# Performance work log

Hardware: AMD Instinct MI355X
Metric: run time of the kernel (lower is better)

## Reference

```python
import jax, jax.numpy as jnp
import numpy as np

EPS = 1e-12  # torch F.normalize default eps


def setup_inputs() -> dict:
    key = jax.random.key(0)
    k1, k2, k3, k4, k5 = jax.random.split(key, 5)
    N, E, D_IN, D_OUT = 100000, 1600000, 128, 128
    features = jax.random.normal(k1, (N, D_IN), dtype=jnp.float32)
    W = jax.random.normal(k2, (D_OUT, D_IN), dtype=jnp.float32) * 0.05
    b = jax.random.normal(k3, (D_OUT,), dtype=jnp.float32) * 0.05
    src = jax.random.randint(k4, (E,), 0, N, dtype=jnp.int32)
    dst = jax.random.randint(k5, (E,), 0, N, dtype=jnp.int32)
    return {"features": features, "W": W, "b": b, "src": src, "dst": dst}


def reference(features, W, b, src, dst):
    N = features.shape[0]
    # sum of features over each node's neighbors: scatter-add messages to dst
    neigh_sum = jax.ops.segment_sum(features[src], dst, num_segments=N)  # [N, D]
    total = jnp.sum(features, axis=0)  # [D]
    # non-neighbor sum (excl. self) + self feature == total - neighbor_sum
    h_NN = total[None, :] - neigh_sum  # [N, D]
    # row-wise L2 normalize (torch F.normalize dim=1)
    norm = jnp.sqrt(jnp.sum(h_NN * h_NN, axis=1, keepdims=True))
    h_norm = h_NN / jnp.maximum(norm, EPS)
    # linear: x @ W.T + b
    return h_norm @ W.T + b
```

## Files before the change

### kernel.cpp

```cpp
#include <hip/hip_runtime.h>
#include <hip/hip_bf16.h>

#define D 128
#define FS_CAP 5120

typedef __bf16 bf16_t;
typedef bf16_t bf16x8 __attribute__((ext_vector_type(8)));
typedef float  f32x4  __attribute__((ext_vector_type(4)));
typedef float  f32x2  __attribute__((ext_vector_type(2)));

__device__ __forceinline__ void atomAddF(float* p, float v) {
    unsafeAtomicAdd(p, v);
}

__device__ __forceinline__ uint2 pack_fp8x8(const float* v) {
    unsigned lo = 0, hi = 0;
    lo = __builtin_amdgcn_cvt_pk_fp8_f32(v[0], v[1], lo, false);
    lo = __builtin_amdgcn_cvt_pk_fp8_f32(v[2], v[3], lo, true);
    hi = __builtin_amdgcn_cvt_pk_fp8_f32(v[4], v[5], hi, false);
    hi = __builtin_amdgcn_cvt_pk_fp8_f32(v[6], v[7], hi, true);
    return make_uint2(lo, hi);
}

__device__ __forceinline__ void acc_fp8x8(uint2 w, float* acc) {
    f32x2 a = __builtin_amdgcn_cvt_pk_f32_fp8(w.x, false);
    f32x2 b = __builtin_amdgcn_cvt_pk_f32_fp8(w.x, true);
    f32x2 c = __builtin_amdgcn_cvt_pk_f32_fp8(w.y, false);
    f32x2 d = __builtin_amdgcn_cvt_pk_f32_fp8(w.y, true);
    acc[0] += a[0]; acc[1] += a[1]; acc[2] += b[0]; acc[3] += b[1];
    acc[4] += c[0]; acc[5] += c[1]; acc[6] += d[0]; acc[7] += d[1];
}

__global__ __launch_bounds__(256) void cvt_colsum_count_kernel(const float* __restrict__ feat,
                                                               uint2* __restrict__ featq,
                                                               float* __restrict__ total,
                                                               const int* __restrict__ dst,
                                                               int* __restrict__ bcount,
                                                               int* __restrict__ chunkhist,
                                                               long long n8, int nE, int NB,
                                                               int echunk) {
    __shared__ float red[4][16][8];
    __shared__ int hist[1024];
    int tid = threadIdx.x, lane = tid & 63, w = tid >> 6;
    for (int i = tid; i < NB; i += 256) hist[i] = 0;
    __syncthreads();
    long long G = (long long)gridDim.x * 256;
    float acc[8];
    #pragma unroll
    for (int e = 0; e < 8; ++e) acc[e] = 0.f;
    int c0 = blockIdx.x * echunk;
    int c1 = c0 + echunk; if (c1 > nE) c1 = nE;
    long long i = (long long)blockIdx.x * 256 + tid;
    int e = c0 + tid;
    while (i < n8 || e < c1) {
        if (i < n8) {
            const float4 a = *(const float4*)&feat[i * 8];
            const float4 b = *(const float4*)&feat[i * 8 + 4];
            float v[8] = {a.x, a.y, a.z, a.w, b.x, b.y, b.z, b.w};
            featq[i] = pack_fp8x8(v);
            acc[0] += a.x; acc[1] += a.y; acc[2] += a.z; acc[3] += a.w;
            acc[4] += b.x; acc[5] += b.y; acc[6] += b.z; acc[7] += b.w;
        }
        if (e < c1) atomicAdd(&hist[dst[e] >> 8], 1);
        i += G; e += 256;
    }
    #pragma unroll
    for (int k = 0; k < 8; ++k) {
        acc[k] += __shfl_xor(acc[k], 16, 64);
        acc[k] += __shfl_xor(acc[k], 32, 64);
    }
    if (lane < 16) {
        #pragma unroll
        for (int k = 0; k < 8; ++k) red[w][lane][k] = acc[k];
    }
    __syncthreads();
    if (tid < 128) {
        int cb = tid >> 3, k = tid & 7;
        float s = red[0][cb][k] + red[1][cb][k] + red[2][cb][k] + red[3][cb][k];
        atomAddF(&total[cb * 8 + k], s);
    }
    int* ch = chunkhist + (size_t)(blockIdx.x >> 2) * 1024;
    for (int k = tid; k < NB; k += 256) {
        int h = hist[k];
        if (h) { atomicAdd(&ch[k], h); atomicAdd(&bcount[k], h); }
    }
}

__global__ __launch_bounds__(1024) void bucket_scatter_kernel(const int* __restrict__ src,
                                                              const int* __restrict__ dst,
                                                              const int* __restrict__ bcount,
                                                              int* __restrict__ bcur_rel,
                                                              int* __restrict__ bbase,
                                                              unsigned* __restrict__ packed,
                                                              const int* __restrict__ chunkhist,
                                                              int nE, int NB, int echunk4) {
    __shared__ int ws[16];
    __shared__ int cur[1024];
    int blk = blockIdx.x;
    int tid = threadIdx.x, lane = tid & 63, w = tid >> 6;

    int v = (tid < NB) ? bcount[tid] : 0;
    int x = v;
    #pragma unroll
    for (int off = 1; off < 64; off <<= 1) {
        int y = __shfl_up(x, off, 64);
        if (lane >= off) x += y;
    }
    if (lane == 63) ws[w] = x;
    __syncthreads();
    if (w == 0 && lane < 16) {
        int s = ws[lane];
        #pragma unroll
        for (int off = 1; off < 16; off <<= 1) {
            int y = __shfl_up(s, off, 64);
            if (lane >= off) s += y;
        }
        ws[lane] = s;
    }
    __syncthreads();
    int base = (w == 0) ? 0 : ws[w - 1];
    int excl = base + x - v;

    if (blk == 0) {
        if (tid < NB) bbase[tid] = excl;
        if (tid == 0) bbase[NB] = nE;
    }
    if (tid < NB) {
        int h = chunkhist[(size_t)blk * 1024 + tid];
        cur[tid] = h ? (excl + atomicAdd(&bcur_rel[tid], h)) : 0;
    }
    __syncthreads();

    int c0 = blk * echunk4;
    int c1 = c0 + echunk4; if (c1 > nE) c1 = nE;
    for (int i = c0 + tid; i < c1; i += 1024) {
        int t = dst[i];
        int b = t >> 8;
        int off = atomicAdd(&cur[b], 1);
        packed[off] = ((unsigned)(t & 255) << 17) | (unsigned)src[i];
    }
}

__global__ __launch_bounds__(1024) void fill_sort_kernel(const unsigned* __restrict__ packed,
                                                         const int* __restrict__ bbase,
                                                         int* __restrict__ ptr,
                                                         int* __restrict__ adj,
                                                         int n, int NB, int nE) {
    __shared__ int cnt[256];
    __shared__ int lcur[256];
    __shared__ int wsum[4];
    __shared__ int pbuf[FS_CAP];
    __shared__ int sbuf[FS_CAP];
    int b = blockIdx.x;
    int tid = threadIdx.x, lane = tid & 63, w = tid >> 6;
    int base = bbase[b], end = bbase[b + 1], m = end - base;
    bool fast = (m <= FS_CAP);
    if (tid < 256) cnt[tid] = 0;
    __syncthreads();
    if (fast) {
        for (int i = tid; i < m; i += 1024) {
            int pv = (int)packed[base + i];
            pbuf[i] = pv;
            atomicAdd(&cnt[pv >> 17], 1);
        }
    } else {
        for (int i = tid; i < m; i += 1024)
            atomicAdd(&cnt[packed[base + i] >> 17], 1);
    }
    __syncthreads();
    int v = 0, x = 0;
    if (tid < 256) {
        v = cnt[tid];
        x = v;
        #pragma unroll
        for (int off = 1; off < 64; off <<= 1) {
            int y = __shfl_up(x, off, 64);
            if (lane >= off) x += y;
        }
        if (lane == 63) wsum[w] = x;
    }
    __syncthreads();
    if (tid < 256) {
        int wb = 0;
        for (int k = 0; k < w; ++k) wb += wsum[k];
        int excl = wb + x - v;
        lcur[tid] = fast ? excl : base + excl;
        int node = b * 256 + tid;
        if (node < n) ptr[node] = base + excl;
    }
    if (b == NB - 1 && tid == 0) ptr[n] = nE;
    __syncthreads();
    if (fast) {
        for (int i = tid; i < m; i += 1024) {
            int pv = pbuf[i];
            int j = pv >> 17;
            int pos = atomicAdd(&lcur[j], 1);
            sbuf[pos] = pv & 0x1FFFF;
        }
        __syncthreads();
        for (int i = tid; i < m; i += 1024)
            adj[base + i] = sbuf[i];
    } else {
        for (int i = tid; i < m; i += 1024) {
            int pv = (int)packed[base + i];
            int j = pv >> 17;
            int pos = atomicAdd(&lcur[j], 1);
            adj[pos] = pv & 0x1FFFF;
        }
    }
}

__global__ __launch_bounds__(256, 4) void gather_mfma_kernel(const uint2* __restrict__ featq,
                                                             const int* __restrict__ ptr,
                                                             const int* __restrict__ adj,
                                                             const float* __restrict__ total,
                                                             const float* __restrict__ W,
                                                             const float* __restrict__ bias,
                                                             float* __restrict__ out,
                                                             int n, int ngroups) {
    __shared__ bf16_t s_hn[2][16][136];

    int tid  = threadIdx.x;
    int lane = tid & 63;
    int w    = tid >> 6;
    int quad = lane >> 4;
    int l16  = lane & 15;

    int n0 = w * 32;
    bf16x8 bfrag[4][2];
    #pragma unroll
    for (int s = 0; s < 4; ++s)
        #pragma unroll
        for (int c = 0; c < 2; ++c) {
            const float* wp = W + (size_t)(n0 + 16 * c + l16) * D + 32 * s + 8 * quad;
            float4 wa = *(const float4*)wp;
            float4 wb = *(const float4*)(wp + 4);
            bf16x8 bf;
            bf[0] = (bf16_t)wa.x; bf[1] = (bf16_t)wa.y; bf[2] = (bf16_t)wa.z; bf[3] = (bf16_t)wa.w;
            bf[4] = (bf16_t)wb.x; bf[5] = (bf16_t)wb.y; bf[6] = (bf16_t)wb.z; bf[7] = (bf16_t)wb.w;
            bfrag[s][c] = bf;
        }
    float bias0 = bias[n0 + l16];
    float bias1 = bias[n0 + 16 + l16];

    int k_node = tid >> 4;
    int d8 = (tid & 15) * 8;
    float tot8[8];
    {
        float4 ta = *(const float4*)&total[d8];
        float4 tb = *(const float4*)&total[d8 + 4];
        tot8[0] = ta.x; tot8[1] = ta.y; tot8[2] = ta.z; tot8[3] = ta.w;
        tot8[4] = tb.x; tot8[5] = tb.y; tot8[6] = tb.z; tot8[7] = tb.w;
    }

    unsigned sliceoff = (unsigned)(tid & 15) * 8;
    unsigned long long fbase = (unsigned long long)featq;
    int pb = 0;
    int gstride = gridDim.x;
    int g = blockIdx.x;

    int p0 = 0, p1 = 0, madj = 0;
    if (g < ngroups) {
        int v = g * 16 + k_node;
        if (v < n) { p0 = ptr[v]; p1 = ptr[v + 1]; }
        if (p0 < p1) { int q = p0 + l16; if (q > p1 - 1) q = p1 - 1; madj = adj[q]; }
    }

    for (; g < ngroups; g += gstride) {
        int gn = g + gstride;
        int np0 = 0, np1 = 0;
        if (gn < ngroups) {
            int vn = gn * 16 + k_node;
            if (vn < n) { np0 = ptr[vn]; np1 = ptr[vn + 1]; }
        }

        float acc8[8];
        #pragma unroll
        for (int e = 0; e < 8; ++e) acc8[e] = 0.f;

        for (int p = p0; p < p1; p += 16) {
            int rem = p1 - p;
            unsigned voff[16];
            #pragma unroll
            for (int i = 0; i < 16; ++i) {
                int idx = __shfl(madj, (lane & 48) + i, 64);
                voff[i] = ((unsigned)idx << 7) | sliceoff;
            }
            uint2 f[16];
            #pragma unroll
            for (int i = 0; i < 16; ++i)
                asm volatile("global_load_dwordx2 %0, %1, %2"
                             : "=v"(f[i]) : "v"(voff[i]), "s"(fbase));
            int adjn = 0, pn = p + 16;
            if (pn < p1) { int q = pn + l16; if (q > p1 - 1) q = p1 - 1; adjn = adj[q]; }
            asm volatile("s_waitcnt vmcnt(8)" ::: "memory");
            __builtin_amdgcn_sched_barrier(0);
            #pragma unroll
            for (int i = 0; i < 8; ++i) if (i < rem) acc_fp8x8(f[i], acc8);
            asm volatile("s_waitcnt vmcnt(0)" ::: "memory");
            __builtin_amdgcn_sched_barrier(0);
            #pragma unroll
            for (int i = 8; i < 16; ++i) if (i < rem) acc_fp8x8(f[i], acc8);
            madj = adjn;
        }

        int v = g * 16 + k_node;
        bool valid = v < n;
        float h8[8], ss = 0.f;
        #pragma unroll
        for (int e = 0; e < 8; ++e) {
            h8[e] = valid ? (tot8[e] - acc8[e]) : 0.f;
            ss = fmaf(h8[e], h8[e], ss);
        }
        ss += __shfl_xor(ss, 1, 64);
        ss += __shfl_xor(ss, 2, 64);
        ss += __shfl_xor(ss, 4, 64);
        ss += __shfl_xor(ss, 8, 64);
        float rinv = 1.0f / fmaxf(sqrtf(ss), 1e-12f);

        bf16x8 hv;
        #pragma unroll
        for (int e = 0; e < 8; ++e) hv[e] = (bf16_t)(h8[e] * rinv);
        *(bf16x8*)&s_hn[pb][k_node][d8] = hv;
        __syncthreads();

        p0 = np0; p1 = np1; madj = 0;
        if (p0 < p1) { int q = p0 + l16; if (q > p1 - 1) q = p1 - 1; madj = adj[q]; }

        f32x4 acc0 = {0.f, 0.f, 0.f, 0.f};
        f32x4 acc1 = {0.f, 0.f, 0.f, 0.f};
        #pragma unroll
        for (int s = 0; s < 4; ++s) {
            bf16x8 a = *(const bf16x8*)&s_hn[pb][l16][32 * s + 8 * quad];
            acc0 = __builtin_amdgcn_mfma_f32_16x16x32_bf16(a, bfrag[s][0], acc0, 0, 0, 0);
            acc1 = __builtin_amdgcn_mfma_f32_16x16x32_bf16(a, bfrag[s][1], acc1, 0, 0, 0);
        }
        #pragma unroll
        for (int r = 0; r < 4; ++r) {
            int row = quad * 4 + r;
            int vr = g * 16 + row;
            if (vr < n) {
                out[(size_t)vr * D + n0 + l16]      = acc0[r] + bias0;
                out[(size_t)vr * D + n0 + 16 + l16] = acc1[r] + bias1;
            }
        }
        pb ^= 1;
    }
}

__global__ __launch_bounds__(128) void col_sum_kernel(const float* __restrict__ feat,
                                                      float* __restrict__ total, int n) {
    int d = threadIdx.x;
    float acc = 0.f;
    for (int r = blockIdx.x; r < n; r += gridDim.x)
        acc += feat[(size_t)r * D + d];
    atomAddF(&total[d], acc);
}

__global__ __launch_bounds__(256) void scatter_kernel(const float* __restrict__ feat,
                                                      const int* __restrict__ src,
                                                      const int* __restrict__ dst,
                                                      float* __restrict__ neigh, int nE) {
    long long nwork = (long long)nE * 64;
    long long stride = (long long)gridDim.x * 256;
    for (long long i = (long long)blockIdx.x * 256 + threadIdx.x; i < nwork; i += stride) {
        int e = (int)(i >> 6);
        int d2 = (int)(i & 63) * 2;
        int s = src[e], t = dst[e];
        const float2 vv = *(const float2*)&feat[(size_t)s * D + d2];
        float* p = &neigh[(size_t)t * D + d2];
        atomAddF(p + 0, vv.x);
        atomAddF(p + 1, vv.y);
    }
}

__global__ __launch_bounds__(256) void finalize_kernel(const float* __restrict__ neigh,
                                                       const float* __restrict__ total,
                                                       const float* __restrict__ W,
                                                       const float* __restrict__ bias,
                                                       float* __restrict__ out,
                                                       int n, int ngroups) {
    __shared__ __hip_bfloat16 Wt[D * D];
    __shared__ __align__(16) float hnt[2][D][4];
    __shared__ float red[2][2][4];
    int tid = threadIdx.x;
    for (int idx = tid; idx < D * D; idx += 256) {
        int j = idx & 127, dd = idx >> 7;
        Wt[idx] = __float2bfloat16(W[(size_t)j * D + dd]);
    }
    int half = tid >> 7, d = tid & 127, wih = (tid >> 6) & 1, lane = tid & 63;
    float bj = bias[d], tot = total[d];
    __syncthreads();
    for (int g = blockIdx.x; g < ngroups; g += gridDim.x) {
        int nb = g * 8 + half * 4;
        float h0=0,h1=0,h2=0,h3=0;
        if (nb+0 < n) h0 = tot - neigh[(size_t)(nb+0)*D + d];
        if (nb+1 < n) h1 = tot - neigh[(size_t)(nb+1)*D + d];
        if (nb+2 < n) h2 = tot - neigh[(size_t)(nb+2)*D + d];
        if (nb+3 < n) h3 = tot - neigh[(size_t)(nb+3)*D + d];
        float s0=h0*h0,s1=h1*h1,s2=h2*h2,s3=h3*h3;
        #pragma unroll
        for (int off = 32; off > 0; off >>= 1) {
            s0 += __shfl_xor(s0, off, 64); s1 += __shfl_xor(s1, off, 64);
            s2 += __shfl_xor(s2, off, 64); s3 += __shfl_xor(s3, off, 64);
        }
        if (lane == 0) { red[half][wih][0]=s0; red[half][wih][1]=s1; red[half][wih][2]=s2; red[half][wih][3]=s3; }
        __syncthreads();
        float rinv[4];
        #pragma unroll
        for (int k = 0; k < 4; ++k)
            rinv[k] = 1.0f / fmaxf(sqrtf(red[half][0][k] + red[half][1][k]), 1e-12f);
        hnt[half][d][0]=h0*rinv[0]; hnt[half][d][1]=h1*rinv[1];
        hnt[half][d][2]=h2*rinv[2]; hnt[half][d][3]=h3*rinv[3];
        __syncthreads();
        float a0=0,a1=0,a2=0,a3=0;
        #pragma unroll 8
        for (int dd = 0; dd < D; ++dd) {
            float4 hn4 = *(const float4*)&hnt[half][dd][0];
            float wv = __bfloat162float(Wt[dd * D + d]);
            a0 = fmaf(hn4.x, wv, a0); a1 = fmaf(hn4.y, wv, a1);
            a2 = fmaf(hn4.z, wv, a2); a3 = fmaf(hn4.w, wv, a3);
        }
        if (nb+0 < n) out[(size_t)(nb+0)*D + d] = a0 + bj;
        if (nb+1 < n) out[(size_t)(nb+1)*D + d] = a1 + bj;
        if (nb+2 < n) out[(size_t)(nb+2)*D + d] = a2 + bj;
        if (nb+3 < n) out[(size_t)(nb+3)*D + d] = a3 + bj;
        __syncthreads();
    }
}

static inline size_t align_up(size_t x, size_t a) { return (x + a - 1) & ~(a - 1); }

extern "C" void kernel_launch(void* const* d_in, const int* in_sizes, int n_in,
                              void* d_out, int out_size, void* d_ws, size_t ws_size,
                              hipStream_t stream) {
    const float* feat = (const float*)d_in[0];
    const float* W    = (const float*)d_in[1];
    const float* bias = (const float*)d_in[2];
    const int*   src  = (const int*)d_in[3];
    const int*   dst  = (const int*)d_in[4];
    float* out = (float*)d_out;

    int n  = in_sizes[0] / D;
    int nE = in_sizes[3];
    int NB = (n + 255) / 256;

    char* wsb = (char*)d_ws;
    size_t o_total  = 0;
    size_t o_bcount = 512;
    size_t o_bcurr  = 512 + 4096;
    size_t o_chist  = o_bcurr + 4096;
    size_t o_bbase  = o_chist + (size_t)128 * 1024 * 4;
    size_t o_ptr    = align_up(o_bbase + 4608, 512);
    size_t o_adj    = align_up(o_ptr + (size_t)4 * (n + 1), 512);
    size_t o_packed = o_adj + (size_t)4 * nE;
    size_t o_featq  = align_up(o_packed + (size_t)4 * nE, 512);
    size_t needNew  = o_featq + (size_t)n * D;

    float*    total  = (float*)(wsb + o_total);
    int*      bcount = (int*)(wsb + o_bcount);
    int*      bcurr  = (int*)(wsb + o_bcurr);
    int*      chist  = (int*)(wsb + o_chist);
    int*      bbase  = (int*)(wsb + o_bbase);
    int*      ptr    = (int*)(wsb + o_ptr);
    int*      adj    = (int*)(wsb + o_adj);
    unsigned* packed = (unsigned*)(wsb + o_packed);
    uint2*    featq  = (uint2*)(wsb + o_featq);

    long long n8 = (long long)n * (D / 8);
    int ngroups16 = (n + 15) / 16;
    int grid16 = (ngroups16 + 1) / 2;
    if (grid16 > 16384) grid16 = 16384;

    bool packOK = (n <= (1 << 17)) && (NB <= 1024);

    if (ws_size >= needNew && packOK) {
        hipMemsetAsync(wsb, 0, o_bbase, stream);
        int echunk = (nE + 511) / 512;
        int echunk4 = echunk * 4;
        cvt_colsum_count_kernel<<<512, 256, 0, stream>>>(feat, featq, total, dst, bcount,
                                                         chist, n8, nE, NB, echunk);
        bucket_scatter_kernel<<<128, 1024, 0, stream>>>(src, dst, bcount, bcurr, bbase,
                                                        packed, chist, nE, NB, echunk4);
        fill_sort_kernel<<<NB, 1024, 0, stream>>>(packed, bbase, ptr, adj, n, NB, nE);
        gather_mfma_kernel<<<grid16, 256, 0, stream>>>(featq, ptr, adj, total, W,
                                                       bias, out, n, ngroups16);
    } else {
        float* neigh = out;
        if (ws_size >= D * sizeof(float))
            hipMemsetAsync(d_ws, 0, D * sizeof(float), stream);
        hipMemsetAsync(neigh, 0, (size_t)out_size * sizeof(float), stream);
        col_sum_kernel<<<512, 128, 0, stream>>>(feat, total, n);
        scatter_kernel<<<16384, 256, 0, stream>>>(feat, src, dst, neigh, nE);
        int ngroups = (n + 7) / 8;
        finalize_kernel<<<2048, 256, 0, stream>>>(neigh, total, W, bias, out, n, ngroups);
    }
}
```

Baseline: 211.5 us.

## Split fused convert/colsum/count kernel into separate count and convert kernels

Splits the combined fp8-conversion, column-sum and dst-bucket histogram kernel into a dedicated bucket_count kernel and a standalone cvt_colsum kernel. The convert kernel now runs with 2048 blocks, the count and scatter kernels with 256 blocks. Each count block writes its own chunk histogram directly instead of four blocks atomically merging into a shared one, so the workspace is rearranged so that chist is no longer covered by the zeroing memset. The goal is to remove the imbalance of the fused loop and the global atomics, at the cost of one extra kernel launch and a larger chunk-histogram buffer.

Result: slower. 248.1 us (+17.3%).

```diff
diff --git a/kernel.cpp b/kernel.cpp
--- a/kernel.cpp
+++ b/kernel.cpp
@@ -31,38 +31,23 @@
     acc[4] += c[0]; acc[5] += c[1]; acc[6] += d[0]; acc[7] += d[1];
 }
 
-__global__ __launch_bounds__(256) void cvt_colsum_count_kernel(const float* __restrict__ feat,
-                                                               uint2* __restrict__ featq,
-                                                               float* __restrict__ total,
-                                                               const int* __restrict__ dst,
-                                                               int* __restrict__ bcount,
-                                                               int* __restrict__ chunkhist,
-                                                               long long n8, int nE, int NB,
-                                                               int echunk) {
+__global__ __launch_bounds__(256) void cvt_colsum_kernel(const float* __restrict__ feat,
+                                                         uint2* __restrict__ featq,
+                                                         float* __restrict__ total,
+                                                         long long n8) {
     __shared__ float red[4][16][8];
-    __shared__ int hist[1024];
     int tid = threadIdx.x, lane = tid & 63, w = tid >> 6;
-    for (int i = tid; i < NB; i += 256) hist[i] = 0;
-    __syncthreads();
     long long G = (long long)gridDim.x * 256;
     float acc[8];
     #pragma unroll
     for (int e = 0; e < 8; ++e) acc[e] = 0.f;
-    int c0 = blockIdx.x * echunk;
-    int c1 = c0 + echunk; if (c1 > nE) c1 = nE;
-    long long i = (long long)blockIdx.x * 256 + tid;
-    int e = c0 + tid;
-    while (i < n8 || e < c1) {
-        if (i < n8) {
-            const float4 a = *(const float4*)&feat[i * 8];
-            const float4 b = *(const float4*)&feat[i * 8 + 4];
-            float v[8] = {a.x, a.y, a.z, a.w, b.x, b.y, b.z, b.w};
-            featq[i] = pack_fp8x8(v);
-            acc[0] += a.x; acc[1] += a.y; acc[2] += a.z; acc[3] += a.w;
-            acc[4] += b.x; acc[5] += b.y; acc[6] += b.z; acc[7] += b.w;
-        }
-        if (e < c1) atomicAdd(&hist[dst[e] >> 8], 1);
-        i += G; e += 256;
+    for (long long i = (long long)blockIdx.x * 256 + tid; i < n8; i += G) {
+        const float4 a = *(const float4*)&feat[i * 8];
+        const float4 b = *(const float4*)&feat[i * 8 + 4];
+        float v[8] = {a.x, a.y, a.z, a.w, b.x, b.y, b.z, b.w};
+        featq[i] = pack_fp8x8(v);
+        acc[0] += a.x; acc[1] += a.y; acc[2] += a.z; acc[3] += a.w;
+        acc[4] += b.x; acc[5] += b.y; acc[6] += b.z; acc[7] += b.w;
     }
     #pragma unroll
     for (int k = 0; k < 8; ++k) {
@@ -79,10 +64,25 @@
         float s = red[0][cb][k] + red[1][cb][k] + red[2][cb][k] + red[3][cb][k];
         atomAddF(&total[cb * 8 + k], s);
     }
-    int* ch = chunkhist + (size_t)(blockIdx.x >> 2) * 1024;
+}
+
+__global__ __launch_bounds__(256) void bucket_count_kernel(const int* __restrict__ dst,
+                                                           int* __restrict__ bcount,
+                                                           int* __restrict__ chunkhist,
+                                                           int nE, int NB, int echunkS) {
+    __shared__ int hist[1024];
+    int tid = threadIdx.x;
+    for (int i = tid; i < NB; i += 256) hist[i] = 0;
+    __syncthreads();
+    int c0 = blockIdx.x * echunkS;
+    int c1 = c0 + echunkS; if (c1 > nE) c1 = nE;
+    for (int i = c0 + tid; i < c1; i += 256) atomicAdd(&hist[dst[i] >> 8], 1);
+    __syncthreads();
+    int* ch = chunkhist + (size_t)blockIdx.x * 1024;
     for (int k = tid; k < NB; k += 256) {
         int h = hist[k];
-        if (h) { atomicAdd(&ch[k], h); atomicAdd(&bcount[k], h); }
+        ch[k] = h;
+        if (h) atomicAdd(&bcount[k], h);
     }
 }
 
@@ -93,7 +93,7 @@
                                                               int* __restrict__ bbase,
                                                               unsigned* __restrict__ packed,
                                                               const int* __restrict__ chunkhist,
-                                                              int nE, int NB, int echunk4) {
+                                                              int nE, int NB, int echunkS) {
     __shared__ int ws[16];
     __shared__ int cur[1024];
     int blk = blockIdx.x;
@@ -131,8 +131,8 @@
     }
     __syncthreads();
 
-    int c0 = blk * echunk4;
-    int c1 = c0 + echunk4; if (c1 > nE) c1 = nE;
+    int c0 = blk * echunkS;
+    int c1 = c0 + echunkS; if (c1 > nE) c1 = nE;
     for (int i = c0 + tid; i < c1; i += 1024) {
         int t = dst[i];
         int b = t >> 8;
@@ -449,9 +449,9 @@
     size_t o_total  = 0;
     size_t o_bcount = 512;
     size_t o_bcurr  = 512 + 4096;
-    size_t o_chist  = o_bcurr + 4096;
-    size_t o_bbase  = o_chist + (size_t)128 * 1024 * 4;
-    size_t o_ptr    = align_up(o_bbase + 4608, 512);
+    size_t o_bbase  = o_bcurr + 4096;
+    size_t o_chist  = align_up(o_bbase + 4608, 512);
+    size_t o_ptr    = o_chist + (size_t)256 * 1024 * 4;
     size_t o_adj    = align_up(o_ptr + (size_t)4 * (n + 1), 512);
     size_t o_packed = o_adj + (size_t)4 * nE;
     size_t o_featq  = align_up(o_packed + (size_t)4 * nE, 512);
@@ -460,8 +460,8 @@
     float*    total  = (float*)(wsb + o_total);
     int*      bcount = (int*)(wsb + o_bcount);
     int*      bcurr  = (int*)(wsb + o_bcurr);
+    int*      bbase  = (int*)(wsb + o_bbase);
     int*      chist  = (int*)(wsb + o_chist);
-    int*      bbase  = (int*)(wsb + o_bbase);
     int*      ptr    = (int*)(wsb + o_ptr);
     int*      adj    = (int*)(wsb + o_adj);
     unsigned* packed = (unsigned*)(wsb + o_packed);
@@ -476,12 +476,11 @@
 
     if (ws_size >= needNew && packOK) {
         hipMemsetAsync(wsb, 0, o_bbase, stream);
-        int echunk = (nE + 511) / 512;
-        int echunk4 = echunk * 4;
-        cvt_colsum_count_kernel<<<512, 256, 0, stream>>>(feat, featq, total, dst, bcount,
-                                                         chist, n8, nE, NB, echunk);
-        bucket_scatter_kernel<<<128, 1024, 0, stream>>>(src, dst, bcount, bcurr, bbase,
-                                                        packed, chist, nE, NB, echunk4);
+        int echunkS = (nE + 255) / 256;
+        bucket_count_kernel<<<256, 256, 0, stream>>>(dst, bcount, chist, nE, NB, echunkS);
+        cvt_colsum_kernel<<<2048, 256, 0, stream>>>(feat, featq, total, n8);
+        bucket_scatter_kernel<<<256, 1024, 0, stream>>>(src, dst, bcount, bcurr, bbase,
+                                                        packed, chist, nE, NB, echunkS);
         fill_sort_kernel<<<NB, 1024, 0, stream>>>(packed, bbase, ptr, adj, n, NB, nE);
         gather_mfma_kernel<<<grid16, 256, 0, stream>>>(featq, ptr, adj, total, W,
                                                        bias, out, n, ngroups16);
```
